# Performance work log

Hardware: AMD Instinct MI355X
Metric: run time of the kernel (lower is better)

The kernel has to match this reference:

```python
import jax, jax.numpy as jnp
import numpy as np

B, S, ENC_UNITS, DEC_UNITS, NUM_UNITS = 64, 2048, 512, 512, 512


def setup_inputs() -> dict:
    key = jax.random.key(0)
    k_h, k_eo, k_w1, k_b1, k_w2, k_b2, k_v, k_bv = jax.random.split(key, 8)
    sd = 0.05
    return {
        "H": jax.random.normal(k_h, (B, DEC_UNITS), dtype=jnp.float32),
        "EO": jax.random.normal(k_eo, (B, S, ENC_UNITS), dtype=jnp.float32),
        "W1": jax.random.normal(k_w1, (ENC_UNITS, NUM_UNITS), dtype=jnp.float32) * sd,
        "b1": jnp.zeros((NUM_UNITS,), dtype=jnp.float32),
        "W2": jax.random.normal(k_w2, (DEC_UNITS, NUM_UNITS), dtype=jnp.float32) * sd,
        "b2": jnp.zeros((NUM_UNITS,), dtype=jnp.float32),
        "V": jax.random.normal(k_v, (NUM_UNITS, 1), dtype=jnp.float32) * sd,
        "bv": jnp.zeros((1,), dtype=jnp.float32),
    }


def reference(H, EO, W1, b1, W2, b2, V, bv):
    # H: [B, D], EO: [B, S, E]
    # score = V(tanh(W1(EO) + W2(H)[:, None, :]))  -> [B, S, 1]
    w1_eo = jnp.einsum("bse,eu->bsu", EO, W1) + b1          # [B, S, U]
    w2_h = (H @ W2 + b2)[:, None, :]                          # [B, 1, U]
    score = jnp.tanh(w1_eo + w2_h) @ V + bv                   # [B, S, 1]
    attention_weights = jax.nn.softmax(score, axis=1)         # [B, S, 1]
    context_vector = jnp.sum(attention_weights * EO, axis=1)  # [B, E]
    return context_vector, attention_weights
```

## Files before the change

### kernel.cpp

```cpp
#include <hip/hip_runtime.h>
#include <hip/hip_bf16.h>


typedef __attribute__((ext_vector_type(8))) short bf16x8;
typedef __attribute__((ext_vector_type(4))) float f32x4;

#define NB 64
#define NS 2048
#define NE 512
#define NU 512

#define ASYNC_CP16(gsrc, ldst)                                               \
  __builtin_amdgcn_global_load_lds(                                          \
      (const __attribute__((address_space(1))) unsigned int*)(gsrc),         \
      (__attribute__((address_space(3))) unsigned int*)(ldst), 16, 0, 0)

__device__ __forceinline__ unsigned short f2bf(float f) {
  union { float f; unsigned int u; } x; x.f = f;
  unsigned int u = x.u;
  unsigned int r = (u + 0x7fffu + ((u >> 16) & 1u)) >> 16;
  return (unsigned short)r;
}

__device__ __forceinline__ float bf2f(short s) {
  union { unsigned int u; float f; } x;
  x.u = ((unsigned int)(unsigned short)s) << 16;
  return x.f;
}

__device__ __forceinline__ float tanh_fast(float x) {
  x = fminf(fmaxf(x, -15.f), 15.f);
  float e = __expf(2.f * x);
  return 1.f - 2.f / (e + 1.f);
}

__global__ __launch_bounds__(256) void pack_w1_kernel(
    const float* __restrict__ W1, unsigned short* __restrict__ W1p) {
  int t = blockIdx.x * 256 + threadIdx.x;
  int k = t >> 9, n = t & 511;
  int kt = k >> 5, kr = k & 31;
  int quad = kr >> 3, j = kr & 7;
  int l = (quad << 4) | (n & 15);
  int nt = n >> 4;
  int dst = ((((nt << 4) + kt) * 64 + l) << 3) + j;
  W1p[dst] = f2bf(W1[t]);
}

__global__ __launch_bounds__(512) void compute_c_kernel(
    const float* __restrict__ H, const float* __restrict__ W2,
    const float* __restrict__ b1, const float* __restrict__ b2,
    float* __restrict__ cvec) {
  const int b = blockIdx.x, u = threadIdx.x;
  __shared__ float hs[512];
  hs[u] = H[(b << 9) + u];
  __syncthreads();
  float s = 0.f;
#pragma unroll 8
  for (int d = 0; d < 512; d++) s = fmaf(hs[d], W2[(d << 9) + u], s);
  cvec[(b << 9) + u] = s + b1[u] + b2[u];
}

__global__ __launch_bounds__(256)
__attribute__((amdgpu_waves_per_eu(2, 2)))
void scores_ctx_kernel(
    const float* __restrict__ EO, const unsigned short* __restrict__ W1p,
    const float* __restrict__ cvec, const float* __restrict__ V,
    float* __restrict__ scores, float* __restrict__ m_ws,
    float* __restrict__ l_ws, float* __restrict__ ck_ws) {
  __shared__ __align__(16) unsigned short Bs[2][16384];
  __shared__ float cs[512], vs[512];
  __shared__ float sc_l[128], p_l[128];
  __shared__ __align__(16) float cpartw[4][512];
  __shared__ float m_sh, lw[2];

  const int tid = threadIdx.x;
  const int b = blockIdx.x >> 4;
  const int strip = blockIdx.x & 15;
  const int s0 = strip << 7;
  const int lane = tid & 63, wave = tid >> 6;
  const int quad = lane >> 4, col = lane & 15;

  const uint4* W1p4 = (const uint4*)W1p;

#pragma unroll
  for (int i = 0; i < 8; i++)
    ASYNC_CP16(W1p4 + i * 256 + wave * 64 + lane,
               ((char*)&Bs[0][0]) + (i * 256 + wave * 64) * 16);

  cs[tid] = cvec[(b << 9) + tid];
  cs[tid + 256] = cvec[(b << 9) + 256 + tid];
  vs[tid] = V[tid];
  vs[tid + 256] = V[256 + tid];

  bf16x8 afrag[2][16];
  {
    const float* r0 =
        EO + ((size_t)(b * NS + s0 + wave * 32 + col)) * NE + quad * 8;
    const float* r1 = r0 + 16 * NE;
#pragma unroll
    for (int kt = 0; kt < 16; kt++) {
      float4 x0 = *(const float4*)(r0 + kt * 32);
      float4 y0 = *(const float4*)(r0 + kt * 32 + 4);
      float4 x1 = *(const float4*)(r1 + kt * 32);
      float4 y1 = *(const float4*)(r1 + kt * 32 + 4);
      union { short s[8]; bf16x8 v; } u0, u1;
      u0.s[0] = (short)f2bf(x0.x); u0.s[1] = (short)f2bf(x0.y);
      u0.s[2] = (short)f2bf(x0.z); u0.s[3] = (short)f2bf(x0.w);
      u0.s[4] = (short)f2bf(y0.x); u0.s[5] = (short)f2bf(y0.y);
      u0.s[6] = (short)f2bf(y0.z); u0.s[7] = (short)f2bf(y0.w);
      u1.s[0] = (short)f2bf(x1.x); u1.s[1] = (short)f2bf(x1.y);
      u1.s[2] = (short)f2bf(x1.z); u1.s[3] = (short)f2bf(x1.w);
      u1.s[4] = (short)f2bf(y1.x); u1.s[5] = (short)f2bf(y1.y);
      u1.s[6] = (short)f2bf(y1.z); u1.s[7] = (short)f2bf(y1.w);
      afrag[0][kt] = u0.v;
      afrag[1][kt] = u1.v;
    }
  }

  __syncthreads();

  float sacc[2][4] = {{0.f, 0.f, 0.f, 0.f}, {0.f, 0.f, 0.f, 0.f}};

  for (int it = 0; it < 16; it++) {
    const int cur = it & 1;
    if (it < 15) {
#pragma unroll
      for (int i = 0; i < 8; i++)
        ASYNC_CP16(W1p4 + (it + 1) * 2048 + i * 256 + wave * 64 + lane,
                   ((char*)&Bs[cur ^ 1][0]) + (i * 256 + wave * 64) * 16);
    }
#pragma unroll
    for (int half = 0; half < 2; half++) {
      const int nt = it * 2 + half;
      f32x4 acc0 = {0.f, 0.f, 0.f, 0.f};
      f32x4 acc1 = {0.f, 0.f, 0.f, 0.f};
      const bf16x8* bp = (const bf16x8*)&Bs[cur][half * 8192];
#pragma unroll
      for (int kt = 0; kt < 16; kt++) {
        bf16x8 bfr = bp[kt * 64 + lane];
        acc0 = __builtin_amdgcn_mfma_f32_16x16x32_bf16(afrag[0][kt], bfr, acc0, 0, 0, 0);
        acc1 = __builtin_amdgcn_mfma_f32_16x16x32_bf16(afrag[1][kt], bfr, acc1, 0, 0, 0);
      }
      int u = (nt << 4) + col;
      float cu = cs[u], vu = vs[u];
#pragma unroll
      for (int r = 0; r < 4; r++) {
        sacc[0][r] += tanh_fast(acc0[r] + cu) * vu;
        sacc[1][r] += tanh_fast(acc1[r] + cu) * vu;
      }
    }
    __syncthreads();
  }

#pragma unroll
  for (int m = 1; m < 16; m <<= 1)
#pragma unroll
    for (int t = 0; t < 2; t++)
#pragma unroll
      for (int r = 0; r < 4; r++)
        sacc[t][r] += __shfl_xor(sacc[t][r], m, 64);

  if (col == 0) {
#pragma unroll
    for (int t = 0; t < 2; t++)
#pragma unroll
      for (int r = 0; r < 4; r++) {
        int row = wave * 32 + t * 16 + quad * 4 + r;
        sc_l[row] = sacc[t][r];
        scores[(size_t)b * NS + s0 + row] = sacc[t][r];
      }
  }
  __syncthreads();

  if (wave == 0) {
    float m0 = fmaxf(sc_l[lane], sc_l[lane + 64]);
#pragma unroll
    for (int off = 32; off; off >>= 1) m0 = fmaxf(m0, __shfl_xor(m0, off, 64));
    if (lane == 0) m_sh = m0;
  }
  __syncthreads();
  const float mstrip = m_sh;

  if (tid < 128) {
    float p = __expf(sc_l[tid] - mstrip);
    p_l[tid] = p;
#pragma unroll
    for (int off = 32; off; off >>= 1) p += __shfl_xor(p, off, 64);
    if (lane == 0) lw[wave] = p;
  }
  __syncthreads();
  if (tid == 0) {
    m_ws[b * 16 + strip] = mstrip;
    l_ws[b * 16 + strip] = lw[0] + lw[1];
  }

  const float p0 = p_l[wave * 32 + col];
  const float p1 = p_l[wave * 32 + 16 + col];
#pragma unroll
  for (int kt = 0; kt < 16; kt++) {
    float v[8];
#pragma unroll
    for (int j = 0; j < 8; j++)
      v[j] = p0 * bf2f(afrag[0][kt][j]) + p1 * bf2f(afrag[1][kt][j]);
#pragma unroll
    for (int m = 1; m < 16; m <<= 1)
#pragma unroll
      for (int j = 0; j < 8; j++) v[j] += __shfl_xor(v[j], m, 64);
    if (col == 0) {
      float* dst = &cpartw[wave][kt * 32 + quad * 8];
      *(float4*)dst = make_float4(v[0], v[1], v[2], v[3]);
      *(float4*)(dst + 4) = make_float4(v[4], v[5], v[6], v[7]);
    }
  }
  __syncthreads();

  {
    float2 s = {0.f, 0.f};
#pragma unroll
    for (int w = 0; w < 4; w++) {
      float2 t = *(const float2*)&cpartw[w][tid * 2];
      s.x += t.x; s.y += t.y;
    }
    *(float2*)&ck_ws[((size_t)(b * 16 + strip)) * 512 + tid * 2] = s;
  }
}

__global__ __launch_bounds__(256) void combine_kernel(
    const float* __restrict__ m_ws, const float* __restrict__ l_ws,
    const float* __restrict__ ck_ws, float* __restrict__ ctx,
    float* __restrict__ w ) {
  const int b = blockIdx.x, tid = threadIdx.x;
  __shared__ float msh[16], lsh[16];
  if (tid < 16) {
    msh[tid] = m_ws[b * 16 + tid];
    lsh[tid] = l_ws[b * 16 + tid];
  }
  __syncthreads();
  float M = msh[0];
#pragma unroll
  for (int k = 1; k < 16; k++) M = fmaxf(M, msh[k]);
  float L = 0.f;
#pragma unroll
  for (int k = 0; k < 16; k++) L += lsh[k] * __expf(msh[k] - M);
  const float invL = 1.f / L;

  float2 acc = {0.f, 0.f};
#pragma unroll
  for (int k = 0; k < 16; k++) {
    float sc = __expf(msh[k] - M);
    float2 t = *(const float2*)&ck_ws[((size_t)(b * 16 + k)) * 512 + tid * 2];
    acc.x += sc * t.x; acc.y += sc * t.y;
  }
  acc.x *= invL; acc.y *= invL;
  *(float2*)&ctx[(b << 9) + tid * 2] = acc;

  float* row = w + (size_t)b * NS;
#pragma unroll
  for (int i = 0; i < 8; i++) {
    float s = row[i * 256 + tid];
    row[i * 256 + tid] = __expf(s - M) * invL;
  }
}

extern "C" void kernel_launch(void* const* d_in, const int* in_sizes, int n_in,
                              void* d_out, int out_size, void* d_ws, size_t ws_size,
                              hipStream_t stream) {
  (void)in_sizes; (void)n_in; (void)out_size; (void)ws_size;
  const float* H  = (const float*)d_in[0];
  const float* EO = (const float*)d_in[1];
  const float* W1 = (const float*)d_in[2];
  const float* b1 = (const float*)d_in[3];
  const float* W2 = (const float*)d_in[4];
  const float* b2 = (const float*)d_in[5];
  const float* V  = (const float*)d_in[6];

  float* out_ctx = (float*)d_out;
  float* out_w   = (float*)d_out + NB * NE;

  char* ws = (char*)d_ws;
  unsigned short* W1p = (unsigned short*)ws;
  float* cvec = (float*)(ws + 512 * 1024);
  float* m_ws = (float*)(ws + 640 * 1024);
  float* l_ws = (float*)(ws + 644 * 1024);
  float* ck_ws = (float*)(ws + 656 * 1024);

  pack_w1_kernel<<<1024, 256, 0, stream>>>(W1, W1p);
  compute_c_kernel<<<NB, 512, 0, stream>>>(H, W2, b1, b2, cvec);
  scores_ctx_kernel<<<1024, 256, 0, stream>>>(EO, W1p, cvec, V, out_w,
                                              m_ws, l_ws, ck_ws);
  combine_kernel<<<NB, 256, 0, stream>>>(m_ws, l_ws, ck_ws, out_ctx, out_w);
}
```

Before: 665.6 us.

## Halve per-block sequence strip to 64 rows and raise occupancy

Each block of the scores/context kernel now covers 64 sequence rows instead of 128, with one 16-row MFMA tile per wave. The grid doubles to 2048 blocks, and the W1 tile streamed through LDS shrinks to one 16-column slice per iteration across 32 iterations. The A-fragment register footprint and LDS use are halved, and the waves-per-EU cap of 2 is replaced by launch_bounds(256,3), aiming for more resident blocks and better latency hiding. In exchange, each W1 tile loaded from LDS is reused over half as many rows, so total W1 traffic and barrier count double, and the combine kernel must merge 32 partials per batch.

```diff
diff --git a/kernel.cpp b/kernel.cpp
--- a/kernel.cpp
+++ b/kernel.cpp
@@ -60,30 +60,28 @@
   cvec[(b << 9) + u] = s + b1[u] + b2[u];
 }
 
-__global__ __launch_bounds__(256)
-__attribute__((amdgpu_waves_per_eu(2, 2)))
-void scores_ctx_kernel(
+__global__ __launch_bounds__(256, 3) void scores_ctx_kernel(
     const float* __restrict__ EO, const unsigned short* __restrict__ W1p,
     const float* __restrict__ cvec, const float* __restrict__ V,
     float* __restrict__ scores, float* __restrict__ m_ws,
     float* __restrict__ l_ws, float* __restrict__ ck_ws) {
-  __shared__ __align__(16) unsigned short Bs[2][16384];
+  __shared__ __align__(16) unsigned short Bs[2][8192];
   __shared__ float cs[512], vs[512];
-  __shared__ float sc_l[128], p_l[128];
-  __shared__ __align__(16) float cpartw[4][512];
-  __shared__ float m_sh, lw[2];
+  __shared__ float sc_l[64], p_l[64];
+  __shared__ __align__(16) float cpart[4][512];
+  __shared__ float m_sh;
 
   const int tid = threadIdx.x;
-  const int b = blockIdx.x >> 4;
-  const int strip = blockIdx.x & 15;
-  const int s0 = strip << 7;
+  const int b = blockIdx.x >> 5;
+  const int strip = blockIdx.x & 31;
+  const int s0 = strip << 6;
   const int lane = tid & 63, wave = tid >> 6;
   const int quad = lane >> 4, col = lane & 15;
 
   const uint4* W1p4 = (const uint4*)W1p;
 
 #pragma unroll
-  for (int i = 0; i < 8; i++)
+  for (int i = 0; i < 4; i++)
     ASYNC_CP16(W1p4 + i * 256 + wave * 64 + lane,
                ((char*)&Bs[0][0]) + (i * 256 + wave * 64) * 16);
 
@@ -92,122 +90,94 @@
   vs[tid] = V[tid];
   vs[tid + 256] = V[256 + tid];
 
-  bf16x8 afrag[2][16];
+  bf16x8 afrag[16];
   {
-    const float* r0 =
-        EO + ((size_t)(b * NS + s0 + wave * 32 + col)) * NE + quad * 8;
-    const float* r1 = r0 + 16 * NE;
+    const float* rp =
+        EO + ((size_t)(b * NS + s0 + wave * 16 + col)) * NE + quad * 8;
 #pragma unroll
     for (int kt = 0; kt < 16; kt++) {
-      float4 x0 = *(const float4*)(r0 + kt * 32);
-      float4 y0 = *(const float4*)(r0 + kt * 32 + 4);
-      float4 x1 = *(const float4*)(r1 + kt * 32);
-      float4 y1 = *(const float4*)(r1 + kt * 32 + 4);
-      union { short s[8]; bf16x8 v; } u0, u1;
-      u0.s[0] = (short)f2bf(x0.x); u0.s[1] = (short)f2bf(x0.y);
-      u0.s[2] = (short)f2bf(x0.z); u0.s[3] = (short)f2bf(x0.w);
-      u0.s[4] = (short)f2bf(y0.x); u0.s[5] = (short)f2bf(y0.y);
-      u0.s[6] = (short)f2bf(y0.z); u0.s[7] = (short)f2bf(y0.w);
-      u1.s[0] = (short)f2bf(x1.x); u1.s[1] = (short)f2bf(x1.y);
-      u1.s[2] = (short)f2bf(x1.z); u1.s[3] = (short)f2bf(x1.w);
-      u1.s[4] = (short)f2bf(y1.x); u1.s[5] = (short)f2bf(y1.y);
-      u1.s[6] = (short)f2bf(y1.z); u1.s[7] = (short)f2bf(y1.w);
-      afrag[0][kt] = u0.v;
-      afrag[1][kt] = u1.v;
-    }
-  }
-
-  __syncthreads();
-
-  float sacc[2][4] = {{0.f, 0.f, 0.f, 0.f}, {0.f, 0.f, 0.f, 0.f}};
-
-  for (int it = 0; it < 16; it++) {
-    const int cur = it & 1;
-    if (it < 15) {
-#pragma unroll
-      for (int i = 0; i < 8; i++)
-        ASYNC_CP16(W1p4 + (it + 1) * 2048 + i * 256 + wave * 64 + lane,
+      float4 x = *(const float4*)(rp + kt * 32);
+      float4 y = *(const float4*)(rp + kt * 32 + 4);
+      union { short s[8]; bf16x8 v; } u0;
+      u0.s[0] = (short)f2bf(x.x); u0.s[1] = (short)f2bf(x.y);
+      u0.s[2] = (short)f2bf(x.z); u0.s[3] = (short)f2bf(x.w);
+      u0.s[4] = (short)f2bf(y.x); u0.s[5] = (short)f2bf(y.y);
+      u0.s[6] = (short)f2bf(y.z); u0.s[7] = (short)f2bf(y.w);
+      afrag[kt] = u0.v;
+    }
+  }
+
+  __syncthreads();
+
+  float sacc[4] = {0.f, 0.f, 0.f, 0.f};
+
+  for (int nt = 0; nt < 32; nt++) {
+    const int cur = nt & 1;
+    if (nt < 31) {
+#pragma unroll
+      for (int i = 0; i < 4; i++)
+        ASYNC_CP16(W1p4 + (nt + 1) * 1024 + i * 256 + wave * 64 + lane,
                    ((char*)&Bs[cur ^ 1][0]) + (i * 256 + wave * 64) * 16);
     }
-#pragma unroll
-    for (int half = 0; half < 2; half++) {
-      const int nt = it * 2 + half;
-      f32x4 acc0 = {0.f, 0.f, 0.f, 0.f};
-      f32x4 acc1 = {0.f, 0.f, 0.f, 0.f};
-      const bf16x8* bp = (const bf16x8*)&Bs[cur][half * 8192];
-#pragma unroll
-      for (int kt = 0; kt < 16; kt++) {
-        bf16x8 bfr = bp[kt * 64 + lane];
-        acc0 = __builtin_amdgcn_mfma_f32_16x16x32_bf16(afrag[0][kt], bfr, acc0, 0, 0, 0);
-        acc1 = __builtin_amdgcn_mfma_f32_16x16x32_bf16(afrag[1][kt], bfr, acc1, 0, 0, 0);
-      }
-      int u = (nt << 4) + col;
-      float cu = cs[u], vu = vs[u];
-#pragma unroll
-      for (int r = 0; r < 4; r++) {
-        sacc[0][r] += tanh_fast(acc0[r] + cu) * vu;
-        sacc[1][r] += tanh_fast(acc1[r] + cu) * vu;
-      }
-    }
+    f32x4 acc = {0.f, 0.f, 0.f, 0.f};
+    const bf16x8* bp = (const bf16x8*)&Bs[cur][0];
+#pragma unroll
+    for (int kt = 0; kt < 16; kt++) {
+      bf16x8 bfr = bp[kt * 64 + lane];
+      acc = __builtin_amdgcn_mfma_f32_16x16x32_bf16(afrag[kt], bfr, acc, 0, 0, 0);
+    }
+    int u = (nt << 4) + col;
+    float cu = cs[u], vu = vs[u];
+#pragma unroll
+    for (int r = 0; r < 4; r++)
+      sacc[r] += tanh_fast(acc[r] + cu) * vu;
     __syncthreads();
   }
 
 #pragma unroll
   for (int m = 1; m < 16; m <<= 1)
 #pragma unroll
-    for (int t = 0; t < 2; t++)
-#pragma unroll
-      for (int r = 0; r < 4; r++)
-        sacc[t][r] += __shfl_xor(sacc[t][r], m, 64);
+    for (int r = 0; r < 4; r++)
+      sacc[r] += __shfl_xor(sacc[r], m, 64);
 
   if (col == 0) {
 #pragma unroll
-    for (int t = 0; t < 2; t++)
-#pragma unroll
-      for (int r = 0; r < 4; r++) {
-        int row = wave * 32 + t * 16 + quad * 4 + r;
-        sc_l[row] = sacc[t][r];
-        scores[(size_t)b * NS + s0 + row] = sacc[t][r];
-      }
+    for (int r = 0; r < 4; r++) {
+      int row = wave * 16 + quad * 4 + r;
+      sc_l[row] = sacc[r];
+      scores[(size_t)b * NS + s0 + row] = sacc[r];
+    }
   }
   __syncthreads();
 
   if (wave == 0) {
-    float m0 = fmaxf(sc_l[lane], sc_l[lane + 64]);
+    float m0 = sc_l[lane];
 #pragma unroll
     for (int off = 32; off; off >>= 1) m0 = fmaxf(m0, __shfl_xor(m0, off, 64));
     if (lane == 0) m_sh = m0;
-  }
-  __syncthreads();
-  const float mstrip = m_sh;
-
-  if (tid < 128) {
-    float p = __expf(sc_l[tid] - mstrip);
-    p_l[tid] = p;
+    float p = __expf(sc_l[lane] - m0);
+    p_l[lane] = p;
 #pragma unroll
     for (int off = 32; off; off >>= 1) p += __shfl_xor(p, off, 64);
-    if (lane == 0) lw[wave] = p;
-  }
-  __syncthreads();
-  if (tid == 0) {
-    m_ws[b * 16 + strip] = mstrip;
-    l_ws[b * 16 + strip] = lw[0] + lw[1];
-  }
-
-  const float p0 = p_l[wave * 32 + col];
-  const float p1 = p_l[wave * 32 + 16 + col];
+    if (lane == 0) {
+      m_ws[b * 32 + strip] = m0;
+      l_ws[b * 32 + strip] = p;
+    }
+  }
+  __syncthreads();
+
+  const float p0 = p_l[wave * 16 + col];
 #pragma unroll
   for (int kt = 0; kt < 16; kt++) {
     float v[8];
 #pragma unroll
-    for (int j = 0; j < 8; j++)
-      v[j] = p0 * bf2f(afrag[0][kt][j]) + p1 * bf2f(afrag[1][kt][j]);
+    for (int j = 0; j < 8; j++) v[j] = p0 * bf2f(afrag[kt][j]);
 #pragma unroll
     for (int m = 1; m < 16; m <<= 1)
 #pragma unroll
       for (int j = 0; j < 8; j++) v[j] += __shfl_xor(v[j], m, 64);
     if (col == 0) {
-      float* dst = &cpartw[wave][kt * 32 + quad * 8];
+      float* dst = &cpart[wave][kt * 32 + quad * 8];
       *(float4*)dst = make_float4(v[0], v[1], v[2], v[3]);
       *(float4*)(dst + 4) = make_float4(v[4], v[5], v[6], v[7]);
     }
@@ -218,10 +188,10 @@
     float2 s = {0.f, 0.f};
 #pragma unroll
     for (int w = 0; w < 4; w++) {
-      float2 t = *(const float2*)&cpartw[w][tid * 2];
+      float2 t = *(const float2*)&cpart[w][tid * 2];
       s.x += t.x; s.y += t.y;
     }
-    *(float2*)&ck_ws[((size_t)(b * 16 + strip)) * 512 + tid * 2] = s;
+    *(float2*)&ck_ws[((size_t)(b * 32 + strip)) * 512 + tid * 2] = s;
   }
 }
 
@@ -230,25 +200,25 @@
     const float* __restrict__ ck_ws, float* __restrict__ ctx,
     float* __restrict__ w ) {
   const int b = blockIdx.x, tid = threadIdx.x;
-  __shared__ float msh[16], lsh[16];
-  if (tid < 16) {
-    msh[tid] = m_ws[b * 16 + tid];
-    lsh[tid] = l_ws[b * 16 + tid];
+  __shared__ float msh[32], lsh[32];
+  if (tid < 32) {
+    msh[tid] = m_ws[b * 32 + tid];
+    lsh[tid] = l_ws[b * 32 + tid];
   }
   __syncthreads();
   float M = msh[0];
 #pragma unroll
-  for (int k = 1; k < 16; k++) M = fmaxf(M, msh[k]);
+  for (int k = 1; k < 32; k++) M = fmaxf(M, msh[k]);
   float L = 0.f;
 #pragma unroll
-  for (int k = 0; k < 16; k++) L += lsh[k] * __expf(msh[k] - M);
+  for (int k = 0; k < 32; k++) L += lsh[k] * __expf(msh[k] - M);
   const float invL = 1.f / L;
 
   float2 acc = {0.f, 0.f};
 #pragma unroll
-  for (int k = 0; k < 16; k++) {
+  for (int k = 0; k < 32; k++) {
     float sc = __expf(msh[k] - M);
-    float2 t = *(const float2*)&ck_ws[((size_t)(b * 16 + k)) * 512 + tid * 2];
+    float2 t = *(const float2*)&ck_ws[((size_t)(b * 32 + k)) * 512 + tid * 2];
     acc.x += sc * t.x; acc.y += sc * t.y;
   }
   acc.x *= invL; acc.y *= invL;
@@ -281,12 +251,12 @@
   unsigned short* W1p = (unsigned short*)ws;
   float* cvec = (float*)(ws + 512 * 1024);
   float* m_ws = (float*)(ws + 640 * 1024);
-  float* l_ws = (float*)(ws + 644 * 1024);
-  float* ck_ws = (float*)(ws + 656 * 1024);
+  float* l_ws = (float*)(ws + 656 * 1024);
+  float* ck_ws = (float*)(ws + 672 * 1024);
 
   pack_w1_kernel<<<1024, 256, 0, stream>>>(W1, W1p);
   compute_c_kernel<<<NB, 512, 0, stream>>>(H, W2, b1, b2, cvec);
-  scores_ctx_kernel<<<1024, 256, 0, stream>>>(EO, W1p, cvec, V, out_w,
+  scores_ctx_kernel<<<2048, 256, 0, stream>>>(EO, W1p, cvec, V, out_w,
                                               m_ws, l_ws, ck_ws);
   combine_kernel<<<NB, 256, 0, stream>>>(m_ws, l_ws, ck_ws, out_ctx, out_w);
 }
```

New measurement: 568.7 us. -14.6%, faster.
